# Kernel tuning notes

Hardware: AMD Instinct MI355X
Metric: run time of the kernel (lower is better)

## Reference

```python
import jax, jax.numpy as jnp
import numpy as np

D_MODEL = 1024
NUM_HEADS = 16
HEAD_DIM = D_MODEL // NUM_HEADS


def setup_inputs() -> dict:
    key = jax.random.key(0)
    k1, k2, k3, k4, k5 = jax.random.split(key, 5)
    x = jax.random.normal(k1, (2, 2048, D_MODEL), dtype=jnp.float32)
    # PyTorch Linear-style params: weight [out, in], bias [out]
    s = 1.0 / np.sqrt(D_MODEL)
    w_qkv = jax.random.uniform(k2, (3 * D_MODEL, D_MODEL), jnp.float32, -s, s)
    b_qkv = jax.random.uniform(k3, (3 * D_MODEL,), jnp.float32, -s, s)
    w_out = jax.random.uniform(k4, (D_MODEL, D_MODEL), jnp.float32, -s, s)
    b_out = jax.random.uniform(k5, (D_MODEL,), jnp.float32, -s, s)
    return {"x": x, "w_qkv": w_qkv, "b_qkv": b_qkv, "w_out": w_out, "b_out": b_out}


def reference(x, w_qkv, b_qkv, w_out, b_out):
    B, S, D = x.shape
    H, hd = NUM_HEADS, HEAD_DIM
    # fused QKV projection: (B,S,3D)
    qkv = jnp.einsum('bsd,ed->bse', x, w_qkv) + b_qkv
    # reshape to (B,S,H,3*hd) then permute to (B,H,S,3*hd) then chunk
    qkv = qkv.reshape(B, S, H, 3 * hd).transpose(0, 2, 1, 3)
    q, k, v = jnp.split(qkv, 3, axis=-1)  # each (B,H,S,hd)
    scores = jnp.einsum('bhqd,bhkd->bhqk', q, k) / np.sqrt(hd).astype(jnp.float32)
    attn = jax.nn.softmax(scores, axis=-1)  # dropout is identity in eval
    out = jnp.einsum('bhqk,bhkd->bhqd', attn, v)
    out = out.transpose(0, 2, 1, 3).reshape(B, S, D)
    return jnp.einsum('bsd,ed->bse', out, w_out) + b_out
```

## Files before the change

kernel.cpp:

```cpp
#include <hip/hip_runtime.h>
#include <hip/hip_bf16.h>

#define D_MODEL 1024
#define S_LEN   2048
#define NBATCH  2
#define NHEADS  16
#define HDIM    64
#define DQKV    3072

typedef short bf16x8 __attribute__((ext_vector_type(8)));
typedef float f32x4  __attribute__((ext_vector_type(4)));
typedef float f32x16 __attribute__((ext_vector_type(16)));
typedef unsigned int u32;

__device__ __forceinline__ unsigned short bf16_rne(float f) {
    unsigned u = __float_as_uint(f);
    return (unsigned short)((u + 0x7FFFu + ((u >> 16) & 1u)) >> 16);
}

__global__ __launch_bounds__(256) void cast_all_bf16(
    const float* __restrict__ x, const float* __restrict__ wq,
    const float* __restrict__ wo, unsigned short* __restrict__ out)
{
    const int n4x = 1048576, n4q = 786432;
    const int total = n4x + n4q + 262144;
    int i = blockIdx.x * blockDim.x + threadIdx.x;
    const int stride = gridDim.x * blockDim.x;
    for (; i < total; i += stride) {
        float4 v;
        if (i < n4x)            v = ((const float4*)x)[i];
        else if (i < n4x + n4q) v = ((const float4*)wq)[i - n4x];
        else                    v = ((const float4*)wo)[i - n4x - n4q];
        ((ushort4*)out)[i] = make_ushort4(bf16_rne(v.x), bf16_rne(v.y),
                                          bf16_rne(v.z), bf16_rne(v.w));
    }
}

__device__ __forceinline__ void gld_lds16(const unsigned short* g, unsigned short* l) {
    __builtin_amdgcn_global_load_lds(
        (const __attribute__((address_space(1))) unsigned int*)g,
        (__attribute__((address_space(3))) unsigned int*)l, 16, 0, 0);
}

__device__ __forceinline__ bf16x8 lds_frag(const unsigned short* base, int row, int e8) {
    int byte = (row << 7) + (e8 << 4);
    byte ^= (row & 7) << 4;
    return *(const bf16x8*)((const char*)base + byte);
}

#define GEMM_CORE(A_, B_, K_)                                                  \
    __shared__ unsigned short sA[2][128 * 64];                                 \
    __shared__ unsigned short sB[2][128 * 64];                                 \
    const int tid  = threadIdx.x;                                              \
    const int lane = tid & 63;                                                 \
    const int wid  = tid >> 6;                                                 \
    const int bm = blockIdx.y * 128, bn = blockIdx.x * 128;                    \
    const int wr = (wid >> 1) * 64, wc = (wid & 1) * 64;                       \
    const int half = wid & 1;                                                  \
    const unsigned short* gsrc = (wid < 2) ? A_ : B_;                          \
    unsigned short* ldst0 = ((wid < 2) ? sA[0] : sB[0]) + half * 4096;         \
    unsigned short* ldst1 = ((wid < 2) ? sA[1] : sB[1]) + half * 4096;         \
    const int brow = ((wid < 2) ? bm : bn) + half * 64;                        \
    const int r8_  = lane >> 3;                                                \
    const int colb_ = ((lane & 7) ^ r8_) << 3;                                 \
    const size_t rowbase = (size_t)(brow + r8_) * K_ + colb_;                  \
    f32x4 acc[4][4];                                                           \
    _Pragma("unroll")                                                          \
    for (int m = 0; m < 4; ++m)                                                \
        _Pragma("unroll")                                                      \
        for (int n = 0; n < 4; ++n)                                            \
            acc[m][n] = f32x4{0.f, 0.f, 0.f, 0.f};                             \
    {                                                                          \
        const unsigned short* g = gsrc + rowbase;                              \
        _Pragma("unroll")                                                      \
        for (int c = 0; c < 8; ++c)                                            \
            gld_lds16(g + (size_t)c * 8 * K_, ldst0 + c * 512);                \
    }                                                                          \
    __syncthreads();                                                           \
    int pb = 0;                                                                \
    for (int k0 = 0; k0 < K_; k0 += 64) {                                      \
        if (k0 + 64 < K_) {                                                    \
            const unsigned short* g = gsrc + rowbase + k0 + 64;                \
            unsigned short* ld = pb ? ldst0 : ldst1;                           \
            _Pragma("unroll")                                                  \
            for (int c = 0; c < 8; ++c)                                        \
                gld_lds16(g + (size_t)c * 8 * K_, ld + c * 512);               \
        }                                                                      \
        const unsigned short* cA = pb ? sA[1] : sA[0];                         \
        const unsigned short* cB = pb ? sB[1] : sB[0];                         \
        _Pragma("unroll")                                                      \
        for (int ks2 = 0; ks2 < 2; ++ks2) {                                    \
            const int e8 = (lane >> 4) + ks2 * 4;                              \
            bf16x8 a[4], b[4];                                                 \
            _Pragma("unroll")                                                  \
            for (int m = 0; m < 4; ++m)                                        \
                a[m] = lds_frag(cA, wr + m * 16 + (lane & 15), e8);            \
            _Pragma("unroll")                                                  \
            for (int n = 0; n < 4; ++n)                                        \
                b[n] = lds_frag(cB, wc + n * 16 + (lane & 15), e8);            \
            _Pragma("unroll")                                                  \
            for (int m = 0; m < 4; ++m)                                        \
                _Pragma("unroll")                                              \
                for (int n = 0; n < 4; ++n)                                    \
                    acc[m][n] = __builtin_amdgcn_mfma_f32_16x16x32_bf16(       \
                        a[m], b[n], acc[m][n], 0, 0, 0);                       \
        }                                                                      \
        __syncthreads();                                                       \
        pb ^= 1;                                                               \
    }

__global__ __launch_bounds__(256) void gemm_mfma_out(
    const unsigned short* __restrict__ A, const unsigned short* __restrict__ B,
    const float* __restrict__ bias, float* __restrict__ C, int M, int N, int K)
{
    GEMM_CORE(A, B, K)
    #pragma unroll
    for (int n = 0; n < 4; ++n) {
        const int col = bn + wc + n * 16 + (lane & 15);
        const float bv = bias[col];
        #pragma unroll
        for (int m = 0; m < 4; ++m) {
            const int row0 = bm + wr + m * 16 + (lane >> 4) * 4;
            #pragma unroll
            for (int j = 0; j < 4; ++j)
                C[(size_t)(row0 + j) * N + col] = acc[m][n][j] + bv;
        }
    }
}

__global__ __launch_bounds__(256) void gemm_mfma_qkv(
    const unsigned short* __restrict__ A, const unsigned short* __restrict__ B,
    const float* __restrict__ bias,
    unsigned short* __restrict__ Qs, unsigned short* __restrict__ Ks,
    unsigned short* __restrict__ Vt, int M, int N, int K)
{
    GEMM_CORE(A, B, K)
    #pragma unroll
    for (int n = 0; n < 4; ++n) {
        const int col = bn + wc + n * 16 + (lane & 15);
        const unsigned head = (unsigned)col / 192u;
        const int c = col - (int)head * 192;
        const int cls = c >> 6;
        const float bv = bias[col];
        #pragma unroll
        for (int m = 0; m < 4; ++m) {
            const int row0 = bm + wr + m * 16 + (lane >> 4) * 4;
            if (cls == 2) {
                const int bb = row0 >> 11, ss = row0 & 2047;
                unsigned short vv[4];
                #pragma unroll
                for (int j = 0; j < 4; ++j) vv[j] = bf16_rne(acc[m][n][j] + bv);
                *(ushort4*)&Vt[((size_t)(bb * NHEADS + head) * HDIM + (c - 128)) * S_LEN + ss] =
                    make_ushort4(vv[0], vv[1], vv[2], vv[3]);
            } else {
                #pragma unroll
                for (int j = 0; j < 4; ++j) {
                    const int row = row0 + j;
                    const int bb = row >> 11, ss = row & 2047;
                    float val = acc[m][n][j] + bv;
                    if (cls == 0) val *= 0.18033688011110918f;
                    const size_t idx = ((size_t)(bb * NHEADS + head) * S_LEN + ss) * HDIM + (c & 63);
                    if (cls == 0) Qs[idx] = bf16_rne(val); else Ks[idx] = bf16_rne(val);
                }
            }
        }
    }
}

__global__ __launch_bounds__(512) void attn_mfma_kernel(
    const unsigned short* __restrict__ Qs, const unsigned short* __restrict__ Ks,
    const unsigned short* __restrict__ Vt, unsigned short* __restrict__ ob)
{
    __shared__ unsigned short smem[2][2][2][4096];

    const int tid  = threadIdx.x;
    const int lane = tid & 63;
    const int wid  = tid >> 6;
    const int wq   = wid & 3;
    const int par  = wid >> 2;
    const int h    = lane >> 5;
    const int qcol = lane & 31;

    const int bid = blockIdx.x;
    const int lb  = (bid & 7) * 64 + (bid >> 3);
    const int qt  = lb & 15;
    const int bh  = lb >> 4;
    const int q0  = qt * 128 + wq * 32;

    bf16x8 qf[4];
    {
        const unsigned short* qr = Qs + ((size_t)bh * S_LEN + q0 + qcol) * HDIM + h * 8;
        #pragma unroll
        for (int ks = 0; ks < 4; ++ks) qf[ks] = *(const bf16x8*)(qr + ks * 16);
    }

    bf16x8 onesv;
    #pragma unroll
    for (int i = 0; i < 8; ++i) onesv[i] = (short)0x3F80;

    const unsigned short* gKV = (wq < 2) ? Ks : Vt;
    const int cls   = wq >> 1;
    const int cbase = (wq & 1) * 4;
    const int r8    = lane >> 3;
    const int colb  = ((lane & 7) ^ r8) << 3;

    float m_run = -1e30f;
    f32x16 accO[2];
    f32x16 accL;
    #pragma unroll
    for (int r = 0; r < 16; ++r) { accO[0][r] = 0.0f; accO[1][r] = 0.0f; accL[r] = 0.0f; }

    #define STAGE(buf, kt)                                                          \
        do {                                                                        \
            unsigned short* pl_ = &smem[buf][par][cls][0];                          \
            if (cls == 0) {                                                         \
                const unsigned short* g_ = gKV + ((size_t)bh * S_LEN + (kt) + r8) * HDIM + colb; \
                _Pragma("unroll")                                                   \
                for (int c_ = 0; c_ < 4; ++c_)                                      \
                    gld_lds16(g_ + (size_t)(cbase + c_) * 8 * HDIM,                 \
                              pl_ + (cbase + c_) * 512);                            \
            } else {                                                                \
                const unsigned short* g_ = gKV + ((size_t)bh * HDIM + r8) * S_LEN + (kt) + colb; \
                _Pragma("unroll")                                                   \
                for (int c_ = 0; c_ < 4; ++c_)                                      \
                    gld_lds16(g_ + (size_t)(cbase + c_) * 8 * S_LEN,                \
                              pl_ + (cbase + c_) * 512);                            \
            }                                                                       \
        } while (0)

    STAGE(0, par * 64);
    __syncthreads();

    int cur = 0;
    for (int it = 0; it < S_LEN / 128; ++it) {
        if (it + 1 < S_LEN / 128) STAGE(cur ^ 1, (it + 1) * 128 + par * 64);

        const unsigned short* cK = &smem[cur][par][0][0];
        const unsigned short* cV = &smem[cur][par][1][0];

        f32x16 accS[2];
        #pragma unroll
        for (int r = 0; r < 16; ++r) { accS[0][r] = 0.0f; accS[1][r] = 0.0f; }

        __builtin_amdgcn_s_setprio(1);
        #pragma unroll
        for (int ks = 0; ks < 4; ++ks) {
            const int e8 = ks * 2 + h;
            #pragma unroll
            for (int mm = 0; mm < 2; ++mm) {
                bf16x8 ak = lds_frag(cK, mm * 32 + qcol, e8);
                accS[mm] = __builtin_amdgcn_mfma_f32_32x32x16_bf16(ak, qf[ks], accS[mm], 0, 0, 0);
            }
        }
        __builtin_amdgcn_s_setprio(0);

        float t16[16];
        #pragma unroll
        for (int i = 0; i < 16; ++i) t16[i] = fmaxf(accS[0][i], accS[1][i]);
        float t8[8];
        #pragma unroll
        for (int i = 0; i < 8; ++i) t8[i] = fmaxf(t16[i], t16[i + 8]);
        float t4[4];
        #pragma unroll
        for (int i = 0; i < 4; ++i) t4[i] = fmaxf(t8[i], t8[i + 4]);
        float mx = fmaxf(fmaxf(t4[0], t4[1]), fmaxf(t4[2], t4[3]));
        mx = fmaxf(mx, __shfl_xor(mx, 32));

        if (!__all(mx <= m_run + 8.0f)) {
            const float mnew = fmaxf(m_run, mx);
            const float corr = __builtin_amdgcn_exp2f(m_run - mnew);
            m_run = mnew;
            #pragma unroll
            for (int r = 0; r < 16; ++r) {
                accO[0][r] *= corr; accO[1][r] *= corr; accL[r] *= corr;
            }
        }

        #pragma unroll
        for (int mm = 0; mm < 2; ++mm)
            #pragma unroll
            for (int r = 0; r < 16; ++r)
                accS[mm][r] = __builtin_amdgcn_exp2f(accS[mm][r] - m_run);

        const bool hib = (h != 0);
        #pragma unroll
        for (int mm = 0; mm < 2; ++mm) {
            u32 wh_[8], sh_[8];
            #pragma unroll
            for (int i = 0; i < 8; ++i) {
                const float pe = accS[mm][2 * i], po = accS[mm][2 * i + 1];
                asm("v_cvt_pk_bf16_f32 %0, %1, %2" : "=v"(wh_[i]) : "v"(pe), "v"(po));
            }
            #pragma unroll
            for (int i = 0; i < 8; ++i) sh_[i] = __shfl_xor(wh_[i], 32);
            #pragma unroll
            for (int cc = 0; cc < 2; ++cc) {
                const int b0 = cc * 4;
                union { u32 w[4]; bf16x8 v; } uh;
                uh.w[0] = hib ? sh_[b0 + 2] : wh_[b0 + 0];
                uh.w[1] = hib ? sh_[b0 + 3] : wh_[b0 + 1];
                uh.w[2] = hib ? wh_[b0 + 2] : sh_[b0 + 0];
                uh.w[3] = hib ? wh_[b0 + 3] : sh_[b0 + 1];
                const int e8 = (mm * 2 + cc) * 2 + h;
                bf16x8 vf0 = lds_frag(cV, qcol, e8);
                bf16x8 vf1 = lds_frag(cV, 32 + qcol, e8);
                accO[0] = __builtin_amdgcn_mfma_f32_32x32x16_bf16(vf0, uh.v, accO[0], 0, 0, 0);
                accO[1] = __builtin_amdgcn_mfma_f32_32x32x16_bf16(vf1, uh.v, accO[1], 0, 0, 0);
                accL    = __builtin_amdgcn_mfma_f32_32x32x16_bf16(onesv, uh.v, accL, 0, 0, 0);
            }
        }

        __syncthreads();
        cur ^= 1;
    }
    #undef STAGE

    const float l_run = accL[0];

    float* mbuf = (float*)&smem[0][0][0][0];
    if (par == 1) {
        float* dst = mbuf + ((size_t)(wq * 64 + lane)) * 35;
        #pragma unroll
        for (int mdc = 0; mdc < 2; ++mdc)
            #pragma unroll
            for (int r = 0; r < 16; ++r) dst[mdc * 16 + r] = accO[mdc][r];
        dst[32] = m_run;
        dst[33] = l_run;
    }
    __syncthreads();
    if (par == 0) {
        const float* src = mbuf + ((size_t)(wq * 64 + lane)) * 35;
        const float m2 = src[32], l2 = src[33];
        const float mt = fmaxf(m_run, m2);
        const float w1 = __builtin_amdgcn_exp2f(m_run - mt);
        const float w2 = __builtin_amdgcn_exp2f(m2 - mt);
        const float inv = 1.0f / (l_run * w1 + l2 * w2);

        const int bb = bh >> 4, hh = bh & 15;
        const int ss = q0 + qcol;
        unsigned short* po = ob + ((size_t)(bb * S_LEN + ss)) * D_MODEL + hh * HDIM;
        #pragma unroll
        for (int mdc = 0; mdc < 2; ++mdc)
            #pragma unroll
            for (int r = 0; r < 16; r += 2) {
                const int d = mdc * 32 + (r & 3) + 8 * (r >> 2) + 4 * h;
                const float v0 = (accO[mdc][r]     * w1 + src[mdc * 16 + r]     * w2) * inv;
                const float v1 = (accO[mdc][r + 1] * w1 + src[mdc * 16 + r + 1] * w2) * inv;
                *(u32*)(po + d) = ((u32)bf16_rne(v1) << 16) | bf16_rne(v0);
            }
    }
}

extern "C" void kernel_launch(void* const* d_in, const int* in_sizes, int n_in,
                              void* d_out, int out_size, void* d_ws, size_t ws_size,
                              hipStream_t stream)
{
    const float* x     = (const float*)d_in[0];
    const float* w_qkv = (const float*)d_in[1];
    const float* b_qkv = (const float*)d_in[2];
    const float* w_out = (const float*)d_in[3];
    const float* b_out = (const float*)d_in[4];
    float* out = (float*)d_out;

    const int M = NBATCH * S_LEN;
    const size_t PL = (size_t)32 * S_LEN * HDIM;

    unsigned short* xb  = (unsigned short*)d_ws;
    unsigned short* wqb = xb  + PL;
    unsigned short* wob = wqb + (size_t)DQKV * D_MODEL;
    unsigned short* Qs  = wob + (size_t)D_MODEL * D_MODEL;
    unsigned short* Ks  = Qs  + PL;
    unsigned short* Vt  = Ks  + PL;
    unsigned short* aob = Vt  + PL;

    dim3 blk(256);
    cast_all_bf16<<<1024, blk, 0, stream>>>(x, w_qkv, w_out, xb);

    gemm_mfma_qkv<<<dim3(DQKV / 128, M / 128), blk, 0, stream>>>(
        xb, wqb, b_qkv, Qs, Ks, Vt, M, DQKV, D_MODEL);

    attn_mfma_kernel<<<dim3(512), dim3(512), 0, stream>>>(Qs, Ks, Vt, aob);

    gemm_mfma_out<<<dim3(D_MODEL / 128, M / 128), blk, 0, stream>>>(
        aob, wob, b_out, out, M, D_MODEL, D_MODEL);
}
```

Before: 126.2 us.

## Software-pipeline attention: overlap next tile's QK^T with current softmax and PV

Restructures the attention inner loop into a two-stage software pipeline: the QK^T MFMAs for tile t+1 are issued before the softmax and PV of tile t, using ping-pong score registers. K gets two LDS buffers and V gets three rotating buffers so loads for tile t+2 can proceed safely. This is meant to hide softmax/exp latency behind MFMA work. It costs more LDS (80KB per block) and more VGPRs for the extra score accumulators, which can reduce occupancy.

```diff
diff --git a/kernel.cpp b/kernel.cpp
--- a/kernel.cpp
+++ b/kernel.cpp
@@ -171,7 +171,7 @@
     const unsigned short* __restrict__ Qs, const unsigned short* __restrict__ Ks,
     const unsigned short* __restrict__ Vt, unsigned short* __restrict__ ob)
 {
-    __shared__ unsigned short smem[2][2][2][4096];
+    __shared__ unsigned short smem[40960];
 
     const int tid  = threadIdx.x;
     const int lane = tid & 63;
@@ -187,6 +187,9 @@
     const int bh  = lb >> 4;
     const int q0  = qt * 128 + wq * 32;
 
+    #define KPL(b) (smem + (par * 2 + (b)) * 4096)
+    #define VPL(b) (smem + 16384 + (par * 3 + (b)) * 4096)
+
     bf16x8 qf[4];
     {
         const unsigned short* qr = Qs + ((size_t)bh * S_LEN + q0 + qcol) * HDIM + h * 8;
@@ -210,9 +213,9 @@
     #pragma unroll
     for (int r = 0; r < 16; ++r) { accO[0][r] = 0.0f; accO[1][r] = 0.0f; accL[r] = 0.0f; }
 
-    #define STAGE(buf, kt)                                                          \
+    #define STAGE(kb, vb, kt)                                                       \
         do {                                                                        \
-            unsigned short* pl_ = &smem[buf][par][cls][0];                          \
+            unsigned short* pl_ = (cls == 0) ? KPL(kb) : VPL(vb);                   \
             if (cls == 0) {                                                         \
                 const unsigned short* g_ = gKV + ((size_t)bh * S_LEN + (kt) + r8) * HDIM + colb; \
                 _Pragma("unroll")                                                   \
@@ -228,96 +231,118 @@
             }                                                                       \
         } while (0)
 
-    STAGE(0, par * 64);
+    #define QKT(SC, kb)                                                             \
+        do {                                                                        \
+            _Pragma("unroll")                                                       \
+            for (int r_ = 0; r_ < 16; ++r_) { SC[0][r_] = 0.0f; SC[1][r_] = 0.0f; } \
+            const unsigned short* cK_ = KPL(kb);                                    \
+            __builtin_amdgcn_s_setprio(1);                                          \
+            _Pragma("unroll")                                                       \
+            for (int ks_ = 0; ks_ < 4; ++ks_) {                                     \
+                const int e8_ = ks_ * 2 + h;                                        \
+                _Pragma("unroll")                                                   \
+                for (int mm_ = 0; mm_ < 2; ++mm_) {                                 \
+                    bf16x8 ak_ = lds_frag(cK_, mm_ * 32 + qcol, e8_);               \
+                    SC[mm_] = __builtin_amdgcn_mfma_f32_32x32x16_bf16(              \
+                        ak_, qf[ks_], SC[mm_], 0, 0, 0);                            \
+                }                                                                   \
+            }                                                                       \
+            __builtin_amdgcn_s_setprio(0);                                          \
+        } while (0)
+
+    #define SOFTMAX_PV(SC, vb)                                                      \
+        do {                                                                        \
+            float t16[16];                                                          \
+            _Pragma("unroll")                                                       \
+            for (int i_ = 0; i_ < 16; ++i_) t16[i_] = fmaxf(SC[0][i_], SC[1][i_]);  \
+            float t8[8];                                                            \
+            _Pragma("unroll")                                                       \
+            for (int i_ = 0; i_ < 8; ++i_) t8[i_] = fmaxf(t16[i_], t16[i_ + 8]);    \
+            float t4[4];                                                            \
+            _Pragma("unroll")                                                       \
+            for (int i_ = 0; i_ < 4; ++i_) t4[i_] = fmaxf(t8[i_], t8[i_ + 4]);      \
+            float mx = fmaxf(fmaxf(t4[0], t4[1]), fmaxf(t4[2], t4[3]));             \
+            mx = fmaxf(mx, __shfl_xor(mx, 32));                                     \
+            if (!__all(mx <= m_run + 8.0f)) {                                       \
+                const float mnew = fmaxf(m_run, mx);                                \
+                const float corr = __builtin_amdgcn_exp2f(m_run - mnew);            \
+                m_run = mnew;                                                       \
+                _Pragma("unroll")                                                   \
+                for (int r_ = 0; r_ < 16; ++r_) {                                   \
+                    accO[0][r_] *= corr; accO[1][r_] *= corr; accL[r_] *= corr;     \
+                }                                                                   \
+            }                                                                       \
+            _Pragma("unroll")                                                       \
+            for (int mm_ = 0; mm_ < 2; ++mm_)                                       \
+                _Pragma("unroll")                                                   \
+                for (int r_ = 0; r_ < 16; ++r_)                                     \
+                    SC[mm_][r_] = __builtin_amdgcn_exp2f(SC[mm_][r_] - m_run);      \
+            const unsigned short* cV_ = VPL(vb);                                    \
+            const bool hib = (h != 0);                                              \
+            _Pragma("unroll")                                                       \
+            for (int mm_ = 0; mm_ < 2; ++mm_) {                                     \
+                u32 wh_[8], sh_[8];                                                 \
+                _Pragma("unroll")                                                   \
+                for (int i_ = 0; i_ < 8; ++i_) {                                    \
+                    const float pe = SC[mm_][2 * i_], po = SC[mm_][2 * i_ + 1];     \
+                    asm("v_cvt_pk_bf16_f32 %0, %1, %2" : "=v"(wh_[i_]) : "v"(pe), "v"(po)); \
+                }                                                                   \
+                _Pragma("unroll")                                                   \
+                for (int i_ = 0; i_ < 8; ++i_) sh_[i_] = __shfl_xor(wh_[i_], 32);   \
+                _Pragma("unroll")                                                   \
+                for (int cc_ = 0; cc_ < 2; ++cc_) {                                 \
+                    const int b0_ = cc_ * 4;                                        \
+                    union { u32 w[4]; bf16x8 v; } uh;                               \
+                    uh.w[0] = hib ? sh_[b0_ + 2] : wh_[b0_ + 0];                    \
+                    uh.w[1] = hib ? sh_[b0_ + 3] : wh_[b0_ + 1];                    \
+                    uh.w[2] = hib ? wh_[b0_ + 2] : sh_[b0_ + 0];                    \
+                    uh.w[3] = hib ? wh_[b0_ + 3] : sh_[b0_ + 1];                    \
+                    const int e8_ = (mm_ * 2 + cc_) * 2 + h;                        \
+                    bf16x8 vf0 = lds_frag(cV_, qcol, e8_);                          \
+                    bf16x8 vf1 = lds_frag(cV_, 32 + qcol, e8_);                     \
+                    accO[0] = __builtin_amdgcn_mfma_f32_32x32x16_bf16(vf0, uh.v, accO[0], 0, 0, 0); \
+                    accO[1] = __builtin_amdgcn_mfma_f32_32x32x16_bf16(vf1, uh.v, accO[1], 0, 0, 0); \
+                    accL    = __builtin_amdgcn_mfma_f32_32x32x16_bf16(onesv, uh.v, accL, 0, 0, 0);  \
+                }                                                                   \
+            }                                                                       \
+        } while (0)
+
+    STAGE(0, 0, par * 64);
+    STAGE(1, 1, 128 + par * 64);
     __syncthreads();
 
-    int cur = 0;
-    for (int it = 0; it < S_LEN / 128; ++it) {
-        if (it + 1 < S_LEN / 128) STAGE(cur ^ 1, (it + 1) * 128 + par * 64);
-
-        const unsigned short* cK = &smem[cur][par][0][0];
-        const unsigned short* cV = &smem[cur][par][1][0];
-
-        f32x16 accS[2];
-        #pragma unroll
-        for (int r = 0; r < 16; ++r) { accS[0][r] = 0.0f; accS[1][r] = 0.0f; }
-
-        __builtin_amdgcn_s_setprio(1);
-        #pragma unroll
-        for (int ks = 0; ks < 4; ++ks) {
-            const int e8 = ks * 2 + h;
-            #pragma unroll
-            for (int mm = 0; mm < 2; ++mm) {
-                bf16x8 ak = lds_frag(cK, mm * 32 + qcol, e8);
-                accS[mm] = __builtin_amdgcn_mfma_f32_32x32x16_bf16(ak, qf[ks], accS[mm], 0, 0, 0);
-            }
+    f32x16 scA[2], scB[2];
+    QKT(scA, 0);
+
+    int vc = 0;
+    for (int it2 = 0; it2 < 8; ++it2) {
+        const int t0 = it2 * 2;
+        const bool last = (it2 == 7);
+
+        if (!last) STAGE(t0 & 1, (vc >= 1) ? vc - 1 : 2, (t0 + 2) * 128 + par * 64);
+        QKT(scB, (t0 + 1) & 1);
+        SOFTMAX_PV(scA, vc);
+        __syncthreads();
+        vc = (vc == 2) ? 0 : vc + 1;
+
+        if (!last) {
+            STAGE((t0 + 1) & 1, (vc >= 1) ? vc - 1 : 2, (t0 + 3) * 128 + par * 64);
+            QKT(scA, t0 & 1);
         }
-        __builtin_amdgcn_s_setprio(0);
-
-        float t16[16];
-        #pragma unroll
-        for (int i = 0; i < 16; ++i) t16[i] = fmaxf(accS[0][i], accS[1][i]);
-        float t8[8];
-        #pragma unroll
-        for (int i = 0; i < 8; ++i) t8[i] = fmaxf(t16[i], t16[i + 8]);
-        float t4[4];
-        #pragma unroll
-        for (int i = 0; i < 4; ++i) t4[i] = fmaxf(t8[i], t8[i + 4]);
-        float mx = fmaxf(fmaxf(t4[0], t4[1]), fmaxf(t4[2], t4[3]));
-        mx = fmaxf(mx, __shfl_xor(mx, 32));
-
-        if (!__all(mx <= m_run + 8.0f)) {
-            const float mnew = fmaxf(m_run, mx);
-            const float corr = __builtin_amdgcn_exp2f(m_run - mnew);
-            m_run = mnew;
-            #pragma unroll
-            for (int r = 0; r < 16; ++r) {
-                accO[0][r] *= corr; accO[1][r] *= corr; accL[r] *= corr;
-            }
-        }
-
-        #pragma unroll
-        for (int mm = 0; mm < 2; ++mm)
-            #pragma unroll
-            for (int r = 0; r < 16; ++r)
-                accS[mm][r] = __builtin_amdgcn_exp2f(accS[mm][r] - m_run);
-
-        const bool hib = (h != 0);
-        #pragma unroll
-        for (int mm = 0; mm < 2; ++mm) {
-            u32 wh_[8], sh_[8];
-            #pragma unroll
-            for (int i = 0; i < 8; ++i) {
-                const float pe = accS[mm][2 * i], po = accS[mm][2 * i + 1];
-                asm("v_cvt_pk_bf16_f32 %0, %1, %2" : "=v"(wh_[i]) : "v"(pe), "v"(po));
-            }
-            #pragma unroll
-            for (int i = 0; i < 8; ++i) sh_[i] = __shfl_xor(wh_[i], 32);
-            #pragma unroll
-            for (int cc = 0; cc < 2; ++cc) {
-                const int b0 = cc * 4;
-                union { u32 w[4]; bf16x8 v; } uh;
-                uh.w[0] = hib ? sh_[b0 + 2] : wh_[b0 + 0];
-                uh.w[1] = hib ? sh_[b0 + 3] : wh_[b0 + 1];
-                uh.w[2] = hib ? wh_[b0 + 2] : sh_[b0 + 0];
-                uh.w[3] = hib ? wh_[b0 + 3] : sh_[b0 + 1];
-                const int e8 = (mm * 2 + cc) * 2 + h;
-                bf16x8 vf0 = lds_frag(cV, qcol, e8);
-                bf16x8 vf1 = lds_frag(cV, 32 + qcol, e8);
-                accO[0] = __builtin_amdgcn_mfma_f32_32x32x16_bf16(vf0, uh.v, accO[0], 0, 0, 0);
-                accO[1] = __builtin_amdgcn_mfma_f32_32x32x16_bf16(vf1, uh.v, accO[1], 0, 0, 0);
-                accL    = __builtin_amdgcn_mfma_f32_32x32x16_bf16(onesv, uh.v, accL, 0, 0, 0);
-            }
-        }
-
+        SOFTMAX_PV(scB, vc);
         __syncthreads();
-        cur ^= 1;
-    }
+        vc = (vc == 2) ? 0 : vc + 1;
+    }
+
     #undef STAGE
+    #undef QKT
+    #undef SOFTMAX_PV
+    #undef KPL
+    #undef VPL
 
     const float l_run = accL[0];
 
-    float* mbuf = (float*)&smem[0][0][0][0];
+    float* mbuf = (float*)smem;
     if (par == 1) {
         float* dst = mbuf + ((size_t)(wq * 64 + lane)) * 35;
         #pragma unroll
```

New measurement: 127.4 us. Within noise of the previous version (+1.0%).
